# Kernel optimization log

Hardware: AMD Instinct MI355X
Metric: run time of the kernel (lower is better)

The kernel has to match this reference:

```python
import jax, jax.numpy as jnp
import numpy as np

B, S, H, E, TOPK = 16384, 64, 256, 8, 2


def setup_inputs() -> dict:
    key = jax.random.key(0)
    k1, k2, k3, k4 = jax.random.split(key, 4)
    x = jax.random.normal(k1, (B, S, H), dtype=jnp.float32)
    xr = jax.random.normal(k2, (B, H), dtype=jnp.float32)
    W_router = jax.random.normal(k3, (H, E), dtype=jnp.float32) * 0.02
    W_experts = jax.random.normal(k4, (E, H, H), dtype=jnp.float32) * 0.02
    b_experts = jnp.zeros((E, H), dtype=jnp.float32)
    return {"x": x, "xr": xr, "W_router": W_router,
            "W_experts": W_experts, "b_experts": b_experts}


def reference(x, xr, W_router, W_experts, b_experts):
    # Routing network: logits [B, E]
    logits = xr @ W_router
    # top-2 expert selection; softmax over the two selected logits (as in torch code)
    top_vals, top_idx = jax.lax.top_k(logits, TOPK)          # [B, 2]
    w = jax.nn.softmax(top_vals, axis=1)                     # [B, 2]
    # Dense gate matrix [B, E]: scatter top-2 weights into expert slots
    gate = jnp.zeros_like(logits).at[jnp.arange(x.shape[0])[:, None], top_idx].add(w)
    # Expert forward: pooled token representation -> per-expert dense tanh
    pooled = x.mean(axis=1)                                  # [B, H]
    h_all = jnp.tanh(jnp.einsum('bh,ehd->bed', pooled, W_experts) + b_experts[None])
    # Weighted scatter-add combine: prediction[b] += w * hidden_states
    prediction = jnp.einsum('be,beh->bh', gate, h_all)       # [B, H]
    return prediction
```

## Files before the change

### kernel.cpp

```cpp
#include <hip/hip_runtime.h>
#include <hip/hip_bf16.h>

constexpr int Bn = 16384;
constexpr int S  = 64;
constexpr int H  = 256;
constexpr int E  = 8;

constexpr int RPB  = 32;
constexpr int CBLK = Bn / RPB;
constexpr int PSTR = H + 8;

constexpr int POOLB = Bn / 4;
constexpr int PREPB = E * 8;

typedef short bf16x8 __attribute__((ext_vector_type(8)));
typedef float f32x4  __attribute__((ext_vector_type(4)));

__device__ __forceinline__ float fast_tanh(float x) {
    const float ex = __expf(2.0f * x);
    return (ex - 1.0f) / (ex + 1.0f);
}

__global__ __launch_bounds__(256) void stage1_kernel(
    const float* __restrict__ x,
    const float* __restrict__ We,
    __hip_bfloat16* __restrict__ pws,
    __hip_bfloat16* __restrict__ Wf)
{
    __shared__ __hip_bfloat16 tile[32][H + 4];
    const int t = threadIdx.x;

    if (blockIdx.x < POOLB) {
        const int row = blockIdx.x * 4 + (t >> 6);
        const int c4  = t & 63;

        const f32x4* xrow = reinterpret_cast<const f32x4*>(x + (size_t)row * (S * H));
        f32x4 a0 = 0.f, a1 = 0.f, a2 = 0.f, a3 = 0.f;
#pragma unroll 16
        for (int s = 0; s < S; s += 4) {
            f32x4 v0 = __builtin_nontemporal_load(xrow + (s + 0) * 64 + c4);
            f32x4 v1 = __builtin_nontemporal_load(xrow + (s + 1) * 64 + c4);
            f32x4 v2 = __builtin_nontemporal_load(xrow + (s + 2) * 64 + c4);
            f32x4 v3 = __builtin_nontemporal_load(xrow + (s + 3) * 64 + c4);
            a0 += v0; a1 += v1; a2 += v2; a3 += v3;
        }
        const f32x4 res = (a0 + a1) + (a2 + a3);
        const float sc = 1.0f / (float)S;
        ushort4 pk;
        {
            __hip_bfloat16 h0 = __float2bfloat16(res[0] * sc);
            __hip_bfloat16 h1 = __float2bfloat16(res[1] * sc);
            __hip_bfloat16 h2 = __float2bfloat16(res[2] * sc);
            __hip_bfloat16 h3 = __float2bfloat16(res[3] * sc);
            pk.x = *reinterpret_cast<unsigned short*>(&h0);
            pk.y = *reinterpret_cast<unsigned short*>(&h1);
            pk.z = *reinterpret_cast<unsigned short*>(&h2);
            pk.w = *reinterpret_cast<unsigned short*>(&h3);
        }
        *reinterpret_cast<ushort4*>(pws + (size_t)row * H + c4 * 4) = pk;
    } else {
        const int bid = blockIdx.x - POOLB;
        const int e   = bid >> 3;
        const int kk  = bid & 7;

        const float* src = We + ((size_t)e * H + kk * 32) * H;
#pragma unroll
        for (int i = 0; i < 8; ++i) {
            const int idx = t + 256 * i;
            const int hh  = idx >> 6;
            const int c4  = idx & 63;
            float4 v = reinterpret_cast<const float4*>(src + (size_t)hh * H)[c4];
            tile[hh][c4 * 4 + 0] = __float2bfloat16(v.x);
            tile[hh][c4 * 4 + 1] = __float2bfloat16(v.y);
            tile[hh][c4 * 4 + 2] = __float2bfloat16(v.z);
            tile[hh][c4 * 4 + 3] = __float2bfloat16(v.w);
        }
        __syncthreads();

#pragma unroll
        for (int i = 0; i < 4; ++i) {
            const int task = i * 256 + t;
            const int nt_  = task >> 6;
            const int l    = task & 63;
            const int hlb  = (l >> 4) * 8;
            const int d    = nt_ * 16 + (l & 15);
            bf16x8 p;
#pragma unroll
            for (int j = 0; j < 8; ++j) {
                __hip_bfloat16 hv = tile[hlb + j][d];
                p[j] = *reinterpret_cast<short*>(&hv);
            }
            reinterpret_cast<bf16x8*>(Wf)[(((size_t)(e * 8 + kk) * 16 + nt_) * 64 + l)] = p;
        }
    }
}

__global__ __launch_bounds__(256, 2) void combine_kernel(
    const __hip_bfloat16* __restrict__ pws,
    const float* __restrict__ xr,
    const float* __restrict__ Wr,
    const float* __restrict__ be,
    const __hip_bfloat16* __restrict__ Wf,
    float* __restrict__ out)
{
    const int b0 = blockIdx.x * RPB;
    const int t  = threadIdx.x;

    __shared__ __hip_bfloat16 pooled[RPB][PSTR];
    __shared__ float logit_s[RPB][E];
    __shared__ float gate_s[RPB][E];

    {
        const __hip_bfloat16* src = pws + (size_t)b0 * H + t * 32;
#pragma unroll
        for (int u = 0; u < 4; ++u) {
            const int g = t * 32 + u * 8;
            bf16x8 v = *reinterpret_cast<const bf16x8*>(src + u * 8);
            *reinterpret_cast<bf16x8*>(&pooled[g >> 8][g & 255]) = v;
        }
    }

    {
        const int r = t >> 3, e = t & 7;
        const float* xrp = xr + (size_t)(b0 + r) * H;
        double acc = 0.0;
#pragma unroll 8
        for (int h = 0; h < H; ++h)
            acc += (double)xrp[h] * (double)Wr[h * E + e];
        logit_s[r][e] = (float)acc;
    }
    __syncthreads();

    if (t < RPB) {
        int i0 = 0; float v0 = logit_s[t][0];
#pragma unroll
        for (int e = 1; e < E; ++e)
            if (logit_s[t][e] > v0) { v0 = logit_s[t][e]; i0 = e; }
        int i1 = -1; float v1 = -3.0e38f;
#pragma unroll
        for (int e = 0; e < E; ++e) {
            if (e == i0) continue;
            if (logit_s[t][e] > v1) { v1 = logit_s[t][e]; i1 = e; }
        }
        const float ex  = expf(v1 - v0);
        const float inv = 1.0f / (1.0f + ex);
#pragma unroll
        for (int e = 0; e < E; ++e) gate_s[t][e] = 0.f;
        gate_s[t][i0] = inv;
        gate_s[t][i1] = ex * inv;
    }
    __syncthreads();

    {
        const int dg = t >> 6;
        const int l  = t & 63;
        const int lr = l & 15;
        const int lq = l >> 4;

        f32x4 oacc[2][4];
#pragma unroll
        for (int m = 0; m < 2; ++m)
#pragma unroll
            for (int n = 0; n < 4; ++n) oacc[m][n] = 0.f;

        const __hip_bfloat16* a0base = &pooled[lr][lq * 8];
        const __hip_bfloat16* a1base = &pooled[16 + lr][lq * 8];
        const bf16x8* wf8 = reinterpret_cast<const bf16x8*>(Wf);

        for (int e = 0; e < E; ++e) {
            f32x4 acc[2][4];
#pragma unroll
            for (int m = 0; m < 2; ++m)
#pragma unroll
                for (int n = 0; n < 4; ++n) acc[m][n] = 0.f;

#pragma unroll
            for (int kk = 0; kk < 8; ++kk) {
                const bf16x8 a0 = *reinterpret_cast<const bf16x8*>(a0base + kk * 32);
                const bf16x8 a1 = *reinterpret_cast<const bf16x8*>(a1base + kk * 32);
                const size_t kb = ((size_t)(e * 8 + kk) * 16 + dg * 4) * 64 + l;
                bf16x8 bfr[4];
#pragma unroll
                for (int n = 0; n < 4; ++n)
                    bfr[n] = wf8[kb + (size_t)n * 64];
#pragma unroll
                for (int n = 0; n < 4; ++n) {
                    acc[0][n] = __builtin_amdgcn_mfma_f32_16x16x32_bf16(a0, bfr[n], acc[0][n], 0, 0, 0);
                    acc[1][n] = __builtin_amdgcn_mfma_f32_16x16x32_bf16(a1, bfr[n], acc[1][n], 0, 0, 0);
                }
            }

            float g[2][4];
#pragma unroll
            for (int m = 0; m < 2; ++m)
#pragma unroll
                for (int j = 0; j < 4; ++j)
                    g[m][j] = gate_s[m * 16 + lq * 4 + j][e];
#pragma unroll
            for (int n = 0; n < 4; ++n) {
                const int d = dg * 64 + n * 16 + lr;
                const float bias = be[e * H + d];
#pragma unroll
                for (int m = 0; m < 2; ++m)
#pragma unroll
                    for (int j = 0; j < 4; ++j)
                        oacc[m][n][j] += g[m][j] * fast_tanh(acc[m][n][j] + bias);
            }
        }

#pragma unroll
        for (int m = 0; m < 2; ++m)
#pragma unroll
            for (int n = 0; n < 4; ++n) {
                const int d = dg * 64 + n * 16 + lr;
#pragma unroll
                for (int j = 0; j < 4; ++j) {
                    const int r = m * 16 + lq * 4 + j;
                    out[(size_t)(b0 + r) * H + d] = oacc[m][n][j];
                }
            }
    }
}

__global__ __launch_bounds__(256) void moe_fused_fallback(
    const float* __restrict__ x, const float* __restrict__ xr,
    const float* __restrict__ Wr, const float* __restrict__ We,
    const float* __restrict__ be, float* __restrict__ out)
{
    const int b = blockIdx.x;
    const int t = threadIdx.x;

    __shared__ float  pooled[H];
    __shared__ float  xr_s[H];
    __shared__ float4 red4[4][64];
    __shared__ float  logits_s[E];
    __shared__ int    sel[2];
    __shared__ float  wsel[2];

    {
        const float4* xrow = reinterpret_cast<const float4*>(x + (size_t)b * S * H);
        const int c4 = t & 63;
        const int sg = t >> 6;
        float4 acc = make_float4(0.f, 0.f, 0.f, 0.f);
#pragma unroll
        for (int i = 0; i < 16; ++i) {
            float4 v = xrow[(sg + 4 * i) * 64 + c4];
            acc.x += v.x; acc.y += v.y; acc.z += v.z; acc.w += v.w;
        }
        red4[sg][c4] = acc;
        xr_s[t] = xr[(size_t)b * H + t];
    }
    __syncthreads();
    {
        const float* r0 = reinterpret_cast<const float*>(&red4[0][0]);
        const float* r1 = reinterpret_cast<const float*>(&red4[1][0]);
        const float* r2 = reinterpret_cast<const float*>(&red4[2][0]);
        const float* r3 = reinterpret_cast<const float*>(&red4[3][0]);
        pooled[t] = (r0[t] + r1[t] + r2[t] + r3[t]) * (1.0f / (float)S);
    }
    if (t < E) {
        double acc = 0.0;
        for (int h = 0; h < H; ++h)
            acc += (double)xr_s[h] * (double)Wr[h * E + t];
        logits_s[t] = (float)acc;
    }
    __syncthreads();
    if (t == 0) {
        int i0 = 0; float v0 = logits_s[0];
        for (int e = 1; e < E; ++e)
            if (logits_s[e] > v0) { v0 = logits_s[e]; i0 = e; }
        int i1 = -1; float v1 = -3.0e38f;
        for (int e = 0; e < E; ++e) {
            if (e == i0) continue;
            if (logits_s[e] > v1) { v1 = logits_s[e]; i1 = e; }
        }
        const float ex = expf(v1 - v0);
        const float inv = 1.0f / (1.0f + ex);
        sel[0] = i0; sel[1] = i1;
        wsel[0] = inv; wsel[1] = ex * inv;
    }
    __syncthreads();
    {
        const int   e0 = sel[0], e1 = sel[1];
        const float w0 = wsel[0], w1 = wsel[1];
        const float* W0 = We + (size_t)e0 * H * H + t;
        const float* W1 = We + (size_t)e1 * H * H + t;
        float a0 = be[e0 * H + t];
        float a1 = be[e1 * H + t];
#pragma unroll 8
        for (int h = 0; h < H; ++h) {
            const float p = pooled[h];
            a0 = fmaf(p, W0[(size_t)h * H], a0);
            a1 = fmaf(p, W1[(size_t)h * H], a1);
        }
        out[(size_t)b * H + t] = w0 * tanhf(a0) + w1 * tanhf(a1);
    }
}

extern "C" void kernel_launch(void* const* d_in, const int* in_sizes, int n_in,
                              void* d_out, int out_size, void* d_ws, size_t ws_size,
                              hipStream_t stream) {
    const float* x  = (const float*)d_in[0];
    const float* xr = (const float*)d_in[1];
    const float* Wr = (const float*)d_in[2];
    const float* We = (const float*)d_in[3];
    const float* be = (const float*)d_in[4];
    float* out = (float*)d_out;

    (void)in_sizes; (void)n_in; (void)out_size;

    const size_t wf_elems = (size_t)E * H * H;
    const size_t need = (wf_elems + (size_t)Bn * H) * sizeof(__hip_bfloat16);
    if (ws_size >= need) {
        __hip_bfloat16* Wf  = (__hip_bfloat16*)d_ws;
        __hip_bfloat16* pws = Wf + wf_elems;
        stage1_kernel<<<POOLB + PREPB, 256, 0, stream>>>(x, We, pws, Wf);
        combine_kernel<<<CBLK, 256, 0, stream>>>(pws, xr, Wr, be, Wf, out);
    } else {
        moe_fused_fallback<<<Bn, 256, 0, stream>>>(x, xr, Wr, We, be, out);
    }
}
```

Measured before the change: 241.4 us.

## Split combine tile across 8 waves and drop nontemporal loads in pooling

After: 256.7 us. +6.4%, slower.

```diff
diff --git a/kernel.cpp b/kernel.cpp
--- a/kernel.cpp
+++ b/kernel.cpp
@@ -6,10 +6,9 @@
 constexpr int H  = 256;
 constexpr int E  = 8;
 
-constexpr int RPB  = 32;
-constexpr int CBLK = Bn / RPB;
-constexpr int PSTR = H + 8;
-
+constexpr int RPB   = 32;
+constexpr int CBLK  = Bn / RPB;
+constexpr int PSTR  = H + 8;
 constexpr int POOLB = Bn / 4;
 constexpr int PREPB = E * 8;
 
@@ -38,10 +37,10 @@
         f32x4 a0 = 0.f, a1 = 0.f, a2 = 0.f, a3 = 0.f;
 #pragma unroll 16
         for (int s = 0; s < S; s += 4) {
-            f32x4 v0 = __builtin_nontemporal_load(xrow + (s + 0) * 64 + c4);
-            f32x4 v1 = __builtin_nontemporal_load(xrow + (s + 1) * 64 + c4);
-            f32x4 v2 = __builtin_nontemporal_load(xrow + (s + 2) * 64 + c4);
-            f32x4 v3 = __builtin_nontemporal_load(xrow + (s + 3) * 64 + c4);
+            f32x4 v0 = xrow[(s + 0) * 64 + c4];
+            f32x4 v1 = xrow[(s + 1) * 64 + c4];
+            f32x4 v2 = xrow[(s + 2) * 64 + c4];
+            f32x4 v3 = xrow[(s + 3) * 64 + c4];
             a0 += v0; a1 += v1; a2 += v2; a3 += v3;
         }
         const f32x4 res = (a0 + a1) + (a2 + a3);
@@ -95,7 +94,7 @@
     }
 }
 
-__global__ __launch_bounds__(256, 2) void combine_kernel(
+__global__ __launch_bounds__(512, 2) void combine_kernel(
     const __hip_bfloat16* __restrict__ pws,
     const float* __restrict__ xr,
     const float* __restrict__ Wr,
@@ -111,16 +110,16 @@
     __shared__ float gate_s[RPB][E];
 
     {
-        const __hip_bfloat16* src = pws + (size_t)b0 * H + t * 32;
-#pragma unroll
-        for (int u = 0; u < 4; ++u) {
-            const int g = t * 32 + u * 8;
+        const __hip_bfloat16* src = pws + (size_t)b0 * H + t * 16;
+#pragma unroll
+        for (int u = 0; u < 2; ++u) {
+            const int g = t * 16 + u * 8;
             bf16x8 v = *reinterpret_cast<const bf16x8*>(src + u * 8);
             *reinterpret_cast<bf16x8*>(&pooled[g >> 8][g & 255]) = v;
         }
     }
 
-    {
+    if (t < RPB * E) {
         const int r = t >> 3, e = t & 7;
         const float* xrp = xr + (size_t)(b0 + r) * H;
         double acc = 0.0;
@@ -152,73 +151,60 @@
     __syncthreads();
 
     {
-        const int dg = t >> 6;
+        const int w  = t >> 6;
         const int l  = t & 63;
+        const int mg = w >> 2;
+        const int dg = w & 3;
         const int lr = l & 15;
         const int lq = l >> 4;
 
-        f32x4 oacc[2][4];
-#pragma unroll
-        for (int m = 0; m < 2; ++m)
-#pragma unroll
-            for (int n = 0; n < 4; ++n) oacc[m][n] = 0.f;
-
-        const __hip_bfloat16* a0base = &pooled[lr][lq * 8];
-        const __hip_bfloat16* a1base = &pooled[16 + lr][lq * 8];
+        f32x4 oacc[4];
+#pragma unroll
+        for (int n = 0; n < 4; ++n) oacc[n] = 0.f;
+
+        const __hip_bfloat16* abase = &pooled[mg * 16 + lr][lq * 8];
         const bf16x8* wf8 = reinterpret_cast<const bf16x8*>(Wf);
 
         for (int e = 0; e < E; ++e) {
-            f32x4 acc[2][4];
-#pragma unroll
-            for (int m = 0; m < 2; ++m)
-#pragma unroll
-                for (int n = 0; n < 4; ++n) acc[m][n] = 0.f;
+            f32x4 acc[4];
+#pragma unroll
+            for (int n = 0; n < 4; ++n) acc[n] = 0.f;
 
 #pragma unroll
             for (int kk = 0; kk < 8; ++kk) {
-                const bf16x8 a0 = *reinterpret_cast<const bf16x8*>(a0base + kk * 32);
-                const bf16x8 a1 = *reinterpret_cast<const bf16x8*>(a1base + kk * 32);
+                const bf16x8 a = *reinterpret_cast<const bf16x8*>(abase + kk * 32);
                 const size_t kb = ((size_t)(e * 8 + kk) * 16 + dg * 4) * 64 + l;
                 bf16x8 bfr[4];
 #pragma unroll
                 for (int n = 0; n < 4; ++n)
                     bfr[n] = wf8[kb + (size_t)n * 64];
 #pragma unroll
-                for (int n = 0; n < 4; ++n) {
-                    acc[0][n] = __builtin_amdgcn_mfma_f32_16x16x32_bf16(a0, bfr[n], acc[0][n], 0, 0, 0);
-                    acc[1][n] = __builtin_amdgcn_mfma_f32_16x16x32_bf16(a1, bfr[n], acc[1][n], 0, 0, 0);
-                }
+                for (int n = 0; n < 4; ++n)
+                    acc[n] = __builtin_amdgcn_mfma_f32_16x16x32_bf16(a, bfr[n], acc[n], 0, 0, 0);
             }
 
-            float g[2][4];
-#pragma unroll
-            for (int m = 0; m < 2; ++m)
-#pragma unroll
-                for (int j = 0; j < 4; ++j)
-                    g[m][j] = gate_s[m * 16 + lq * 4 + j][e];
+            float g[4];
+#pragma unroll
+            for (int j = 0; j < 4; ++j) g[j] = gate_s[mg * 16 + lq * 4 + j][e];
 #pragma unroll
             for (int n = 0; n < 4; ++n) {
                 const int d = dg * 64 + n * 16 + lr;
                 const float bias = be[e * H + d];
 #pragma unroll
-                for (int m = 0; m < 2; ++m)
-#pragma unroll
-                    for (int j = 0; j < 4; ++j)
-                        oacc[m][n][j] += g[m][j] * fast_tanh(acc[m][n][j] + bias);
+                for (int j = 0; j < 4; ++j)
+                    oacc[n][j] += g[j] * fast_tanh(acc[n][j] + bias);
             }
         }
 
 #pragma unroll
-        for (int m = 0; m < 2; ++m)
-#pragma unroll
-            for (int n = 0; n < 4; ++n) {
-                const int d = dg * 64 + n * 16 + lr;
-#pragma unroll
-                for (int j = 0; j < 4; ++j) {
-                    const int r = m * 16 + lq * 4 + j;
-                    out[(size_t)(b0 + r) * H + d] = oacc[m][n][j];
-                }
+        for (int n = 0; n < 4; ++n) {
+            const int d = dg * 64 + n * 16 + lr;
+#pragma unroll
+            for (int j = 0; j < 4; ++j) {
+                const int r = mg * 16 + lq * 4 + j;
+                out[(size_t)(b0 + r) * H + d] = oacc[n][j];
             }
+        }
     }
 }
 
@@ -315,7 +301,7 @@
         __hip_bfloat16* Wf  = (__hip_bfloat16*)d_ws;
         __hip_bfloat16* pws = Wf + wf_elems;
         stage1_kernel<<<POOLB + PREPB, 256, 0, stream>>>(x, We, pws, Wf);
-        combine_kernel<<<CBLK, 256, 0, stream>>>(pws, xr, Wr, be, Wf, out);
+        combine_kernel<<<CBLK, 512, 0, stream>>>(pws, xr, Wr, be, Wf, out);
     } else {
         moe_fused_fallback<<<Bn, 256, 0, stream>>>(x, xr, Wr, We, be, out);
     }
```
